# Kernel optimization log

Measured on AMD Instinct MI355X. Metric: run time of the kernel, lower is better.

The kernel has to match this reference:

```python
import jax, jax.numpy as jnp
import numpy as np

# Config constants (HNet300MConfig)
D = 1536          # d_model
H = 12            # n_heads // 2 used by chunk_attention
MAXC = 256        # max_chunks
MAXSEQ = 1024     # max_seq_length (size_embedding rows)
THRESH = 0.85     # boundary_threshold
B, S = 8, 1024


def setup_inputs() -> dict:
    key = jax.random.key(0)
    ks = jax.random.split(key, 10)
    def nrm(k, shape, scale=0.02):
        return jax.random.normal(k, shape, dtype=jnp.float32) * scale
    return {
        "x": jax.random.normal(ks[0], (B, S, D), dtype=jnp.float32),
        "boundaries": jax.random.uniform(ks[1], (B, S), dtype=jnp.float32),
        # nn.MultiheadAttention params
        "in_proj_w": nrm(ks[2], (3 * D, D)),
        "in_proj_b": jnp.zeros((3 * D,), jnp.float32),
        "out_w": nrm(ks[3], (D, D)),
        "out_b": jnp.zeros((D,), jnp.float32),
        # chunk_processor: Linear(D,2D) -> GELU -> Linear(2D,D) -> LayerNorm
        "w1": nrm(ks[4], (2 * D, D)),
        "b1": jnp.zeros((2 * D,), jnp.float32),
        "w2": nrm(ks[5], (D, 2 * D)),
        "b2": jnp.zeros((D,), jnp.float32),
        "ln_g": jnp.ones((D,), jnp.float32),
        "ln_b": jnp.zeros((D,), jnp.float32),
        "pos_enc": nrm(ks[6], (1, MAXC, D)),         # chunk_pos_encoding
        "size_emb": nrm(ks[7], (MAXSEQ, D), 1.0),    # size_embedding table
    }


def reference(x, boundaries, in_proj_w, in_proj_b, out_w, out_b,
              w1, b1, w2, b2, ln_g, ln_b, pos_enc, size_emb):
    dh = D // H
    # Chunk structure: boundary positions start chunks; seg_id = #boundaries up to
    # and including this token, minus 1. Tokens before the first boundary (seg=-1)
    # belong to no chunk. Final chunk runs from last boundary to seq end.
    is_b = boundaries > THRESH                                   # [B,S]
    seg = jnp.cumsum(is_b.astype(jnp.int32), axis=1) - 1         # [B,S]
    valid = seg >= 0

    # Per-chunk self-attention == full MHA with a block-diagonal mask.
    qkv = x @ in_proj_w.T + in_proj_b                            # [B,S,3D]
    q, k, v = jnp.split(qkv, 3, axis=-1)
    heads = lambda t: t.reshape(B, S, H, dh).transpose(0, 2, 1, 3)  # [B,H,S,dh]
    q, k, v = heads(q), heads(k), heads(v)
    scores = jnp.einsum('bhid,bhjd->bhij', q, k) / jnp.sqrt(jnp.float32(dh))
    blk = (seg[:, :, None] == seg[:, None, :]) & valid[:, :, None]  # [B,S,S]
    scores = jnp.where(blk[:, None], scores, jnp.float32(-1e9))
    attn = jax.nn.softmax(scores, axis=-1)
    ctx = jnp.einsum('bhij,bhjd->bhid', attn, v)
    ctx = ctx.transpose(0, 2, 1, 3).reshape(B, S, D)
    attn_out = ctx @ out_w.T + out_b                             # [B,S,D]

    # Ragged mean-pool per chunk (chunks beyond max_chunks are truncated;
    # tokens with seg=-1 or seg>=MAXC go to a dump bucket).
    seg_c = jnp.where(valid & (seg < MAXC), seg, MAXC)
    flat_seg = (seg_c + jnp.arange(B, dtype=jnp.int32)[:, None] * (MAXC + 1)).reshape(-1)
    sums = jax.ops.segment_sum(attn_out.reshape(-1, D), flat_seg,
                               num_segments=B * (MAXC + 1))
    cnts = jax.ops.segment_sum(jnp.ones((B * S,), jnp.float32), flat_seg,
                               num_segments=B * (MAXC + 1))
    sums = sums.reshape(B, MAXC + 1, D)[:, :MAXC]                # [B,MAXC,D]
    cnts = cnts.reshape(B, MAXC + 1)[:, :MAXC]                   # [B,MAXC]
    mean = sums / jnp.maximum(cnts, 1.0)[..., None]              # 0 for empty chunks

    # Size embedding added per non-empty chunk; empty (padding) chunks stay zero.
    lengths = cnts.astype(jnp.int32)
    size_idx = jnp.minimum(lengths, MAXSEQ - 1)
    size_vec = size_emb[size_idx] * (lengths > 0)[..., None].astype(jnp.float32)

    chunks = mean + size_vec + pos_enc                           # [B,MAXC,D]

    # chunk_processor (dropout inactive at inference)
    h = chunks @ w1.T + b1
    h = jax.nn.gelu(h, approximate=False)
    h = h @ w2.T + b2
    mu = jnp.mean(h, axis=-1, keepdims=True)
    var = jnp.mean((h - mu) ** 2, axis=-1, keepdims=True)
    out = (h - mu) / jnp.sqrt(var + 1e-5) * ln_g + ln_b
    return out
```

## Files before the change

kernel.cpp:

```cpp
#include <hip/hip_runtime.h>
#include <math.h>

#define NB 8
#define SEQ 1024
#define DM 1536
#define NHEAD 12
#define DHEAD 128
#define MAXC 256
#define QKVN 4608
#define THRESH 0.85f

typedef unsigned short u16;
typedef __attribute__((ext_vector_type(8))) __bf16 bf16x8;
typedef __attribute__((ext_vector_type(4))) float f32x4;

struct __align__(4) U2 { u16 x, y; };
struct __align__(8) U4 { u16 x, y, z, w; };

__device__ __forceinline__ float bf2f(u16 u) {
  union { unsigned i; float f; } c; c.i = ((unsigned)u) << 16; return c.f;
}
__device__ __forceinline__ u16 f2bf(float f) {
  union { float f; unsigned i; } c; c.f = f;
  unsigned r = c.i + 0x7FFFu + ((c.i >> 16) & 1u);
  return (u16)(r >> 16);
}

__global__ __launch_bounds__(256) void cvt5_bf16_kernel(
    const float* __restrict__ i0, u16* __restrict__ o0, int n0,
    const float* __restrict__ i1, u16* __restrict__ o1, int n1,
    const float* __restrict__ i2, u16* __restrict__ o2, int n2,
    const float* __restrict__ i3, u16* __restrict__ o3, int n3,
    const float* __restrict__ i4, u16* __restrict__ o4, int n4) {
  const int stride = gridDim.x * blockDim.x;
  const int t0 = blockIdx.x * blockDim.x + threadIdx.x;
  const float* ins[5] = {i0, i1, i2, i3, i4};
  u16* outs[5] = {o0, o1, o2, o3, o4};
  const int ns[5] = {n0, n1, n2, n3, n4};
#pragma unroll
  for (int a = 0; a < 5; ++a) {
    const float* in = ins[a];
    u16* out = outs[a];
    for (int i = t0; i < ns[a]; i += stride) {
      float4 f = ((const float4*)in)[i];
      U4 u; u.x = f2bf(f.x); u.y = f2bf(f.y); u.z = f2bf(f.z); u.w = f2bf(f.w);
      ((U4*)out)[i] = u;
    }
  }
}

__global__ __launch_bounds__(64) void segment_kernel(
    const float* __restrict__ bnd, int* __restrict__ nchunks,
    int* __restrict__ starts, int* __restrict__ lens) {
  const int b = blockIdx.x;
  const int lane = threadIdx.x;
  int running = 0;
  for (int g = 0; g < SEQ / 64; ++g) {
    int s = g * 64 + lane;
    bool isb = bnd[b * SEQ + s] > THRESH;
    unsigned long long mask = __ballot(isb ? 1 : 0);
    int excl = __popcll(mask & ((1ULL << lane) - 1ULL));
    if (isb) {
      int c = running + excl;
      if (c <= MAXC) starts[b * (MAXC + 1) + c] = s;
    }
    running += __popcll(mask);
  }
  if (lane == 0) nchunks[b] = running;
  __syncthreads();
  int ncl = min(running, MAXC);
  for (int c = lane; c < MAXC; c += 64) {
    int v = 0;
    if (c < ncl) {
      int st = starts[b * (MAXC + 1) + c];
      int en = (c + 1 < running) ? starts[b * (MAXC + 1) + c + 1] : SEQ;
      v = en - st;
    }
    lens[b * MAXC + c] = v;
  }
}

__global__ __launch_bounds__(512, 2) void gemm256_kernel(
    const u16* __restrict__ A, const u16* __restrict__ B,
    const int M, const int N, const int K,
    const float* __restrict__ bias, u16* __restrict__ outB) {
  __shared__ __align__(16) u16 lds[3][2][8192];
  const int tid = threadIdx.x;
  const int wid = tid >> 6;
  const int lane = tid & 63;
  const int cpx = gridDim.x >> 3;
  const int bid = ((int)blockIdx.x & 7) * cpx + ((int)blockIdx.x >> 3);
  const int NX = N >> 8;
  const int row0 = (bid / NX) << 8;
  const int col0 = (bid % NX) << 8;

  const int wr = wid >> 2;
  const int wc = wid & 3;
  const int rr = lane & 15;
  const int kg = lane >> 4;
  const int cw = rr * 4 + kg;
  const int slot = cw ^ ((cw >> 3) & 7);
  int srow[2], sk8[2];
#pragma unroll
  for (int i = 0; i < 2; ++i) {
    const int s = i * 512 + tid;
    const int g = s >> 6, c = s & 63;
    const int gch = c ^ ((c >> 3) & 7);
    srow[i] = g * 16 + (gch >> 2);
    sk8[i] = gch & 3;
  }

  const int NT = K >> 5;

#define STAGE_A(t)                                                            \
  {                                                                           \
    const int _b = (t) % 3;                                                   \
    const int _kb = (t) << 5;                                                 \
    _Pragma("unroll") for (int i = 0; i < 2; ++i) {                           \
      u16* ga = const_cast<u16*>(A) + (size_t)(row0 + srow[i]) * K + _kb +    \
                sk8[i] * 8;                                                   \
      __builtin_amdgcn_global_load_lds(                                       \
          (__attribute__((address_space(1))) void*)ga,                        \
          (__attribute__((address_space(3))) void*)&lds[_b][0]                \
              [(i * 512 + wid * 64) * 8], 16, 0, 0);                          \
    }                                                                         \
  }
#define STAGE_B(t)                                                            \
  {                                                                           \
    const int _b = (t) % 3;                                                   \
    const int _kb = (t) << 5;                                                 \
    _Pragma("unroll") for (int i = 0; i < 2; ++i) {                           \
      u16* gb = const_cast<u16*>(B) + (size_t)(col0 + srow[i]) * K + _kb +    \
                sk8[i] * 8;                                                   \
      __builtin_amdgcn_global_load_lds(                                       \
          (__attribute__((address_space(1))) void*)gb,                        \
          (__attribute__((address_space(3))) void*)&lds[_b][1]                \
              [(i * 512 + wid * 64) * 8], 16, 0, 0);                          \
    }                                                                         \
  }

  f32x4 acc[8][4] = {};

  STAGE_A(0); STAGE_B(0);
  STAGE_A(1); STAGE_B(1);
  asm volatile("s_waitcnt vmcnt(4)" ::: "memory");
  __builtin_amdgcn_s_barrier();

  for (int t = 0; t < NT; ++t) {
    const int buf = t % 3;
    bf16x8 af[8], bf[4];
#pragma unroll
    for (int m = 0; m < 8; ++m)
      af[m] = *(const bf16x8*)&lds[buf][0][((wr * 8 + m) * 64 + slot) * 8];
#pragma unroll
    for (int n = 0; n < 4; ++n)
      bf[n] = *(const bf16x8*)&lds[buf][1][((wc * 4 + n) * 64 + slot) * 8];
    if (t + 2 < NT) { STAGE_A(t + 2); STAGE_B(t + 2); }
    __builtin_amdgcn_s_barrier();
    asm volatile("s_waitcnt lgkmcnt(0)" ::: "memory");
    __builtin_amdgcn_sched_barrier(0);
    __builtin_amdgcn_s_setprio(1);
#pragma unroll
    for (int m = 0; m < 8; ++m)
#pragma unroll
      for (int n = 0; n < 4; ++n)
        acc[m][n] = __builtin_amdgcn_mfma_f32_16x16x32_bf16(af[m], bf[n], acc[m][n], 0, 0, 0);
    __builtin_amdgcn_s_setprio(0);
    if (t + 2 < NT) {
      asm volatile("s_waitcnt vmcnt(4)" ::: "memory");
    } else if (t + 1 < NT) {
      asm volatile("s_waitcnt vmcnt(0)" ::: "memory");
    }
    __builtin_amdgcn_s_barrier();
  }
#undef STAGE_A
#undef STAGE_B

#pragma unroll
  for (int m = 0; m < 8; ++m) {
#pragma unroll
    for (int n = 0; n < 4; ++n) {
      const int col = col0 + wc * 64 + n * 16 + rr;
      const float bs = bias[col];
#pragma unroll
      for (int j = 0; j < 4; ++j) {
        const int row = row0 + wr * 128 + m * 16 + (lane >> 4) * 4 + j;
        outB[(size_t)row * N + col] = f2bf(acc[m][n][j] + bs);
      }
    }
  }
}

template <int MODE>
__global__ __launch_bounds__(256) void gemm_bf16_kernel(
    const u16* __restrict__ A, const u16* __restrict__ B,
    const int M, const int N, const int K,
    const float* __restrict__ bias,
    u16* __restrict__ outB, float* __restrict__ outF,
    const int* __restrict__ lens, const float* __restrict__ semb,
    const float* __restrict__ pos) {
  __shared__ __align__(16) u16 As[128 * 32];
  __shared__ __align__(16) u16 Bs[128 * 32];
  const int tid = threadIdx.x;
  const int wave = tid >> 6;
  const int lane = tid & 63;
  const int row0 = blockIdx.y * 128;
  const int col0 = blockIdx.x * 128;
  const int wm = (wave >> 1) * 64;
  const int wn = (wave & 1) * 64;
  const int gch = lane ^ ((lane >> 3) & 7);
  const int sr = gch >> 2;
  const int sc = (gch & 3) * 8;
  const int rr = lane & 15;
  const int kg = lane >> 4;
  const int cwant = rr * 4 + kg;
  const int slot = cwant ^ ((cwant >> 3) & 7);
  f32x4 acc[4][4] = {};

  for (int k0 = 0; k0 < K; k0 += 32) {
    __syncthreads();
#pragma unroll
    for (int t = 0; t < 2; ++t) {
      const int li = wave * 2 + t;
      u16* ga = const_cast<u16*>(A) + (size_t)(row0 + li * 16 + sr) * K + (k0 + sc);
      u16* gb = const_cast<u16*>(B) + (size_t)(col0 + li * 16 + sr) * K + (k0 + sc);
      __builtin_amdgcn_global_load_lds(
          (__attribute__((address_space(1))) void*)ga,
          (__attribute__((address_space(3))) void*)(As + li * 512), 16, 0, 0);
      __builtin_amdgcn_global_load_lds(
          (__attribute__((address_space(1))) void*)gb,
          (__attribute__((address_space(3))) void*)(Bs + li * 512), 16, 0, 0);
    }
    __syncthreads();
    bf16x8 af[4], bfr[4];
#pragma unroll
    for (int m = 0; m < 4; ++m)
      af[m] = *(const bf16x8*)(As + ((wm >> 4) + m) * 512 + slot * 8);
#pragma unroll
    for (int n = 0; n < 4; ++n)
      bfr[n] = *(const bf16x8*)(Bs + ((wn >> 4) + n) * 512 + slot * 8);
#pragma unroll
    for (int m = 0; m < 4; ++m)
#pragma unroll
      for (int n = 0; n < 4; ++n)
        acc[m][n] = __builtin_amdgcn_mfma_f32_16x16x32_bf16(af[m], bfr[n], acc[m][n], 0, 0, 0);
  }

  const int rg = (lane >> 4) * 4;
#pragma unroll
  for (int m = 0; m < 4; ++m) {
#pragma unroll
    for (int n = 0; n < 4; ++n) {
      const int col = col0 + wn + n * 16 + rr;
#pragma unroll
      for (int j = 0; j < 4; ++j) {
        const int row = row0 + wm + m * 16 + rg + j;
        float v = acc[m][n][j];
        if (MODE == 2) {
          const int len = lens[row];
          float val = 0.f;
          if (len > 0) {
            const int si = len < 1023 ? len : 1023;
            val = v + bias[col] + semb[(size_t)si * DM + col];
          }
          val += pos[(size_t)(row & (MAXC - 1)) * DM + col];
          outB[(size_t)row * N + col] = f2bf(val);
        } else if (MODE == 3) {
          float z = v + bias[col];
          float gel = 0.5f * z * (1.f + erff(z * 0.70710678118654752440f));
          outB[(size_t)row * N + col] = f2bf(gel);
        } else {
          outF[(size_t)row * N + col] = v + bias[col];
        }
      }
    }
  }
}

__global__ __launch_bounds__(64) void chunk_attn_kernel(
    const u16* __restrict__ qkv, const int* __restrict__ nchunks,
    const int* __restrict__ starts, const int* __restrict__ lens,
    u16* __restrict__ pooled) {
  __shared__ float g_lds[SEQ];
  const int h = blockIdx.x;
  const int c = blockIdx.y;
  const int b = blockIdx.z;
  const int lane = threadIdx.x;
  const int nc = min(nchunks[b], MAXC);
  u16* prow = pooled + ((size_t)(b * MAXC + c)) * DM + h * DHEAD;
  if (c >= nc) {
    U2 z; z.x = 0; z.y = 0;
    *(U2*)(prow + lane * 2) = z;
    return;
  }
  const int s0 = starts[b * (MAXC + 1) + c];
  const int L = lens[b * MAXC + c];
  const u16* Qb = qkv + ((size_t)(b * SEQ + s0)) * QKVN + h * DHEAD;
  const u16* Kb = Qb + DM;
  const u16* Vb = Qb + 2 * DM;

  const int col = lane & 15;
  const int grp = lane >> 4;
  const float scale = 0.08838834764831845f;

  float a0 = 0.f, a1 = 0.f;

  if (L <= 16) {
    const int rc = col < L ? col : (L - 1);
    bf16x8 qf[4], kf[4];
#pragma unroll
    for (int s = 0; s < 4; ++s) {
      qf[s] = *(const bf16x8*)(Qb + (size_t)rc * QKVN + s * 32 + grp * 8);
      kf[s] = *(const bf16x8*)(Kb + (size_t)rc * QKVN + s * 32 + grp * 8);
    }
    f32x4 sc = {0.f, 0.f, 0.f, 0.f};
#pragma unroll
    for (int s = 0; s < 4; ++s)
      sc = __builtin_amdgcn_mfma_f32_16x16x32_bf16(qf[s], kf[s], sc, 0, 0, 0);
    const bool kvalid = col < L;
    float g = 0.f;
#pragma unroll
    for (int j = 0; j < 4; ++j) {
      float sj = sc[j] * scale;
      float mv = kvalid ? sj : -3e38f;
      mv = fmaxf(mv, __shfl_xor(mv, 1));
      mv = fmaxf(mv, __shfl_xor(mv, 2));
      mv = fmaxf(mv, __shfl_xor(mv, 4));
      mv = fmaxf(mv, __shfl_xor(mv, 8));
      float pv = kvalid ? __expf(sj - mv) : 0.f;
      float dv = pv;
      dv += __shfl_xor(dv, 1);
      dv += __shfl_xor(dv, 2);
      dv += __shfl_xor(dv, 4);
      dv += __shfl_xor(dv, 8);
      const bool rv = (grp * 4 + j) < L;
      g += rv ? pv / dv : 0.f;
    }
    g += __shfl_xor(g, 16);
    g += __shfl_xor(g, 32);
    for (int j = 0; j < L; ++j) {
      float gj = __shfl(g, j);
      U2 vv = *(const U2*)(Vb + (size_t)j * QKVN + lane * 2);
      a0 += gj * bf2f(vv.x);
      a1 += gj * bf2f(vv.y);
    }
  } else {
    float* gw = g_lds;
    for (int j = lane; j < L; j += 64) gw[j] = 0.f;
    const int NT = (L + 15) >> 4;
    for (int qt = 0; qt < NT; ++qt) {
      const int qr = qt * 16 + col;
      const int qrc = qr < L ? qr : (L - 1);
      bf16x8 qf[4];
#pragma unroll
      for (int s = 0; s < 4; ++s)
        qf[s] = *(const bf16x8*)(Qb + (size_t)qrc * QKVN + s * 32 + grp * 8);

      float m[4] = {-3e38f, -3e38f, -3e38f, -3e38f};
      float den[4] = {0.f, 0.f, 0.f, 0.f};
      for (int kt = 0; kt < NT; ++kt) {
        const int kr = kt * 16 + col;
        const bool kvalid = kr < L;
        const int krc = kvalid ? kr : (L - 1);
        f32x4 sc = {0.f, 0.f, 0.f, 0.f};
#pragma unroll
        for (int s = 0; s < 4; ++s) {
          bf16x8 kf = *(const bf16x8*)(Kb + (size_t)krc * QKVN + s * 32 + grp * 8);
          sc = __builtin_amdgcn_mfma_f32_16x16x32_bf16(qf[s], kf, sc, 0, 0, 0);
        }
#pragma unroll
        for (int j = 0; j < 4; ++j) {
          float sj = sc[j] * scale;
          float mv = kvalid ? sj : -3e38f;
          mv = fmaxf(mv, __shfl_xor(mv, 1));
          mv = fmaxf(mv, __shfl_xor(mv, 2));
          mv = fmaxf(mv, __shfl_xor(mv, 4));
          mv = fmaxf(mv, __shfl_xor(mv, 8));
          float mn = fmaxf(m[j], mv);
          float pv = kvalid ? __expf(sj - mn) : 0.f;
          pv += __shfl_xor(pv, 1);
          pv += __shfl_xor(pv, 2);
          pv += __shfl_xor(pv, 4);
          pv += __shfl_xor(pv, 8);
          den[j] = den[j] * __expf(m[j] - mn) + pv;
          m[j] = mn;
        }
      }
      float inv[4];
#pragma unroll
      for (int j = 0; j < 4; ++j) {
        const bool rv = (qt * 16 + grp * 4 + j) < L;
        inv[j] = rv ? 1.f / den[j] : 0.f;
      }
      for (int kt = 0; kt < NT; ++kt) {
        const int kr = kt * 16 + col;
        const bool kvalid = kr < L;
        const int krc = kvalid ? kr : (L - 1);
        f32x4 sc = {0.f, 0.f, 0.f, 0.f};
#pragma unroll
        for (int s = 0; s < 4; ++s) {
          bf16x8 kf = *(const bf16x8*)(Kb + (size_t)krc * QKVN + s * 32 + grp * 8);
          sc = __builtin_amdgcn_mfma_f32_16x16x32_bf16(qf[s], kf, sc, 0, 0, 0);
        }
        float colsum = 0.f;
#pragma unroll
        for (int j = 0; j < 4; ++j)
          colsum += __expf(sc[j] * scale - m[j]) * inv[j];
        colsum += __shfl_xor(colsum, 16);
        colsum += __shfl_xor(colsum, 32);
        if (grp == 0 && kvalid) gw[kt * 16 + col] += colsum;
      }
    }
    for (int j = 0; j < L; ++j) {
      float gj = gw[j];
      U2 vv = *(const U2*)(Vb + (size_t)j * QKVN + lane * 2);
      a0 += gj * bf2f(vv.x);
      a1 += gj * bf2f(vv.y);
    }
  }
  const float invL = 1.f / (float)L;
  U2 r; r.x = f2bf(a0 * invL); r.y = f2bf(a1 * invL);
  *(U2*)(prow + lane * 2) = r;
}

__global__ __launch_bounds__(256) void ln_kernel(
    const float* __restrict__ h2, const float* __restrict__ gamma,
    const float* __restrict__ beta, float* __restrict__ out) {
  const int row = blockIdx.x;
  const float* x = h2 + (size_t)row * DM;
  float* o = out + (size_t)row * DM;
  const int tid = threadIdx.x;
  float v[6];
  float s = 0.f;
#pragma unroll
  for (int i = 0; i < 6; ++i) { v[i] = x[tid + i * 256]; s += v[i]; }
  __shared__ float red[8];
#pragma unroll
  for (int off = 32; off; off >>= 1) s += __shfl_xor(s, off);
  if ((tid & 63) == 0) red[tid >> 6] = s;
  __syncthreads();
  const float mu = (red[0] + red[1] + red[2] + red[3]) * (1.f / (float)DM);
  float vs = 0.f;
#pragma unroll
  for (int i = 0; i < 6; ++i) { float d = v[i] - mu; vs += d * d; }
#pragma unroll
  for (int off = 32; off; off >>= 1) vs += __shfl_xor(vs, off);
  __shared__ float red2[8];
  if ((tid & 63) == 0) red2[tid >> 6] = vs;
  __syncthreads();
  const float var = (red2[0] + red2[1] + red2[2] + red2[3]) * (1.f / (float)DM);
  const float inv = rsqrtf(var + 1e-5f);
#pragma unroll
  for (int i = 0; i < 6; ++i) {
    const int cidx = tid + i * 256;
    o[cidx] = (v[i] - mu) * inv * gamma[cidx] + beta[cidx];
  }
}

extern "C" void kernel_launch(void* const* d_in, const int* in_sizes, int n_in,
                              void* d_out, int out_size, void* d_ws, size_t ws_size,
                              hipStream_t stream) {
  const float* x    = (const float*)d_in[0];
  const float* bnd  = (const float*)d_in[1];
  const float* wqkv = (const float*)d_in[2];
  const float* bqkv = (const float*)d_in[3];
  const float* wout = (const float*)d_in[4];
  const float* bout = (const float*)d_in[5];
  const float* w1   = (const float*)d_in[6];
  const float* b1   = (const float*)d_in[7];
  const float* w2   = (const float*)d_in[8];
  const float* b2   = (const float*)d_in[9];
  const float* lng  = (const float*)d_in[10];
  const float* lnb  = (const float*)d_in[11];
  const float* pos  = (const float*)d_in[12];
  const float* semb = (const float*)d_in[13];
  float* out = (float*)d_out;

  char* ws = (char*)d_ws;
  size_t off = 0;
  auto alloc = [&](size_t bytes) -> char* {
    char* p = ws + off;
    off += (bytes + 255) & ~(size_t)255;
    return p;
  };
  u16* x_bf    = (u16*)alloc((size_t)NB * SEQ * DM * 2);
  u16* wqkv_bf = (u16*)alloc((size_t)3 * DM * DM * 2);
  u16* wout_bf = (u16*)alloc((size_t)DM * DM * 2);
  u16* w1_bf   = (u16*)alloc((size_t)2 * DM * DM * 2);
  u16* w2_bf   = (u16*)alloc((size_t)2 * DM * DM * 2);
  u16* qkv_bf  = (u16*)alloc((size_t)NB * SEQ * QKVN * 2);
  int* nchunks = (int*)alloc(NB * 4);
  int* starts  = (int*)alloc(NB * (MAXC + 1) * 4);
  int* lens    = (int*)alloc(NB * MAXC * 4);
  u16* pooled  = (u16*)alloc((size_t)NB * MAXC * DM * 2);
  u16* chunks  = (u16*)alloc((size_t)NB * MAXC * DM * 2);
  u16* h1      = (u16*)alloc((size_t)NB * MAXC * 2 * DM * 2);
  float* h2    = (float*)alloc((size_t)NB * MAXC * DM * 4);
  (void)ws_size; (void)in_sizes; (void)n_in; (void)out_size;

  cvt5_bf16_kernel<<<2048, 256, 0, stream>>>(
      x, x_bf, NB * SEQ * DM / 4,
      wqkv, wqkv_bf, 3 * DM * DM / 4,
      wout, wout_bf, DM * DM / 4,
      w1, w1_bf, 2 * DM * DM / 4,
      w2, w2_bf, 2 * DM * DM / 4);

  segment_kernel<<<NB, 64, 0, stream>>>(bnd, nchunks, starts, lens);

  gemm256_kernel<<<(NB * SEQ / 256) * (QKVN / 256), 512, 0, stream>>>(
      x_bf, wqkv_bf, NB * SEQ, QKVN, DM, bqkv, qkv_bf);

  chunk_attn_kernel<<<dim3(NHEAD, MAXC, NB), 64, 0, stream>>>(
      qkv_bf, nchunks, starts, lens, pooled);

  gemm_bf16_kernel<2><<<dim3(DM / 128, NB * MAXC / 128), 256, 0, stream>>>(
      pooled, wout_bf, NB * MAXC, DM, DM, bout, chunks, nullptr, lens, semb, pos);

  gemm_bf16_kernel<3><<<dim3(2 * DM / 128, NB * MAXC / 128), 256, 0, stream>>>(
      chunks, w1_bf, NB * MAXC, 2 * DM, DM, b1, h1, nullptr, nullptr, nullptr, nullptr);

  gemm_bf16_kernel<4><<<dim3(DM / 128, NB * MAXC / 128), 256, 0, stream>>>(
      h1, w2_bf, NB * MAXC, DM, 2 * DM, b2, nullptr, h2, nullptr, nullptr, nullptr);

  ln_kernel<<<NB * MAXC, 256, 0, stream>>>(h2, lng, lnb, out);
}
```

Measured before the change: 396.4 us.

## Deepen GEMM prefetch pipelines and vectorize chunk-attention V accumulation

The 256-tile GEMM goes from three to four LDS stages with a prefetch distance of three and drops one barrier per iteration. The 128-tile GEMM gains double buffering so the next k-slab loads while MFMAs run. The chunk-attention V accumulation now has each half-wave take alternate rows with 4-wide loads, then combines the halves with a shuffle. LDS use rises (4x32KB per block in the 256 kernel), which may cut occupancy below the launch-bound target of 2 blocks, and removing the barrier may expose a reuse race on the buffer.

```diff
diff --git a/kernel.cpp b/kernel.cpp
--- a/kernel.cpp
+++ b/kernel.cpp
@@ -84,7 +84,7 @@
     const u16* __restrict__ A, const u16* __restrict__ B,
     const int M, const int N, const int K,
     const float* __restrict__ bias, u16* __restrict__ outB) {
-  __shared__ __align__(16) u16 lds[3][2][8192];
+  __shared__ __align__(16) u16 lds[4][2][8192];
   const int tid = threadIdx.x;
   const int wid = tid >> 6;
   const int lane = tid & 63;
@@ -112,26 +112,19 @@
 
   const int NT = K >> 5;
 
-#define STAGE_A(t)                                                            \
+#define STAGE(t)                                                              \
   {                                                                           \
-    const int _b = (t) % 3;                                                   \
+    const int _b = (t) & 3;                                                   \
     const int _kb = (t) << 5;                                                 \
     _Pragma("unroll") for (int i = 0; i < 2; ++i) {                           \
       u16* ga = const_cast<u16*>(A) + (size_t)(row0 + srow[i]) * K + _kb +    \
+                sk8[i] * 8;                                                   \
+      u16* gb = const_cast<u16*>(B) + (size_t)(col0 + srow[i]) * K + _kb +    \
                 sk8[i] * 8;                                                   \
       __builtin_amdgcn_global_load_lds(                                       \
           (__attribute__((address_space(1))) void*)ga,                        \
           (__attribute__((address_space(3))) void*)&lds[_b][0]                \
               [(i * 512 + wid * 64) * 8], 16, 0, 0);                          \
-    }                                                                         \
-  }
-#define STAGE_B(t)                                                            \
-  {                                                                           \
-    const int _b = (t) % 3;                                                   \
-    const int _kb = (t) << 5;                                                 \
-    _Pragma("unroll") for (int i = 0; i < 2; ++i) {                           \
-      u16* gb = const_cast<u16*>(B) + (size_t)(col0 + srow[i]) * K + _kb +    \
-                sk8[i] * 8;                                                   \
       __builtin_amdgcn_global_load_lds(                                       \
           (__attribute__((address_space(1))) void*)gb,                        \
           (__attribute__((address_space(3))) void*)&lds[_b][1]                \
@@ -141,13 +134,12 @@
 
   f32x4 acc[8][4] = {};
 
-  STAGE_A(0); STAGE_B(0);
-  STAGE_A(1); STAGE_B(1);
-  asm volatile("s_waitcnt vmcnt(4)" ::: "memory");
+  STAGE(0); STAGE(1); STAGE(2);
+  asm volatile("s_waitcnt vmcnt(8)" ::: "memory");
   __builtin_amdgcn_s_barrier();
 
   for (int t = 0; t < NT; ++t) {
-    const int buf = t % 3;
+    const int buf = t & 3;
     bf16x8 af[8], bf[4];
 #pragma unroll
     for (int m = 0; m < 8; ++m)
@@ -155,8 +147,7 @@
 #pragma unroll
     for (int n = 0; n < 4; ++n)
       bf[n] = *(const bf16x8*)&lds[buf][1][((wc * 4 + n) * 64 + slot) * 8];
-    if (t + 2 < NT) { STAGE_A(t + 2); STAGE_B(t + 2); }
-    __builtin_amdgcn_s_barrier();
+    if (t + 3 < NT) STAGE(t + 3);
     asm volatile("s_waitcnt lgkmcnt(0)" ::: "memory");
     __builtin_amdgcn_sched_barrier(0);
     __builtin_amdgcn_s_setprio(1);
@@ -166,15 +157,16 @@
       for (int n = 0; n < 4; ++n)
         acc[m][n] = __builtin_amdgcn_mfma_f32_16x16x32_bf16(af[m], bf[n], acc[m][n], 0, 0, 0);
     __builtin_amdgcn_s_setprio(0);
-    if (t + 2 < NT) {
+    if (t + 3 < NT) {
+      asm volatile("s_waitcnt vmcnt(8)" ::: "memory");
+    } else if (t + 2 < NT) {
       asm volatile("s_waitcnt vmcnt(4)" ::: "memory");
     } else if (t + 1 < NT) {
       asm volatile("s_waitcnt vmcnt(0)" ::: "memory");
     }
     __builtin_amdgcn_s_barrier();
   }
-#undef STAGE_A
-#undef STAGE_B
+#undef STAGE
 
 #pragma unroll
   for (int m = 0; m < 8; ++m) {
@@ -199,8 +191,8 @@
     u16* __restrict__ outB, float* __restrict__ outF,
     const int* __restrict__ lens, const float* __restrict__ semb,
     const float* __restrict__ pos) {
-  __shared__ __align__(16) u16 As[128 * 32];
-  __shared__ __align__(16) u16 Bs[128 * 32];
+  __shared__ __align__(16) u16 As[2][128 * 32];
+  __shared__ __align__(16) u16 Bs[2][128 * 32];
   const int tid = threadIdx.x;
   const int wave = tid >> 6;
   const int lane = tid & 63;
@@ -215,36 +207,54 @@
   const int kg = lane >> 4;
   const int cwant = rr * 4 + kg;
   const int slot = cwant ^ ((cwant >> 3) & 7);
+  const int NT = K >> 5;
   f32x4 acc[4][4] = {};
 
-  for (int k0 = 0; k0 < K; k0 += 32) {
-    __syncthreads();
-#pragma unroll
-    for (int t = 0; t < 2; ++t) {
-      const int li = wave * 2 + t;
-      u16* ga = const_cast<u16*>(A) + (size_t)(row0 + li * 16 + sr) * K + (k0 + sc);
-      u16* gb = const_cast<u16*>(B) + (size_t)(col0 + li * 16 + sr) * K + (k0 + sc);
-      __builtin_amdgcn_global_load_lds(
-          (__attribute__((address_space(1))) void*)ga,
-          (__attribute__((address_space(3))) void*)(As + li * 512), 16, 0, 0);
-      __builtin_amdgcn_global_load_lds(
-          (__attribute__((address_space(1))) void*)gb,
-          (__attribute__((address_space(3))) void*)(Bs + li * 512), 16, 0, 0);
-    }
-    __syncthreads();
+#define STAGE128(t, bb)                                                       \
+  {                                                                           \
+    const int _k = (t) << 5;                                                  \
+    _Pragma("unroll") for (int tt = 0; tt < 2; ++tt) {                        \
+      const int li = wave * 2 + tt;                                           \
+      u16* ga = const_cast<u16*>(A) + (size_t)(row0 + li * 16 + sr) * K +     \
+                _k + sc;                                                      \
+      u16* gb = const_cast<u16*>(B) + (size_t)(col0 + li * 16 + sr) * K +     \
+                _k + sc;                                                      \
+      __builtin_amdgcn_global_load_lds(                                       \
+          (__attribute__((address_space(1))) void*)ga,                        \
+          (__attribute__((address_space(3))) void*)(As[bb] + li * 512), 16,   \
+          0, 0);                                                              \
+      __builtin_amdgcn_global_load_lds(                                       \
+          (__attribute__((address_space(1))) void*)gb,                        \
+          (__attribute__((address_space(3))) void*)(Bs[bb] + li * 512), 16,   \
+          0, 0);                                                              \
+    }                                                                         \
+  }
+
+  STAGE128(0, 0);
+  asm volatile("s_waitcnt vmcnt(0)" ::: "memory");
+  __builtin_amdgcn_s_barrier();
+
+  for (int t = 0; t < NT; ++t) {
+    const int cb = t & 1;
     bf16x8 af[4], bfr[4];
 #pragma unroll
     for (int m = 0; m < 4; ++m)
-      af[m] = *(const bf16x8*)(As + ((wm >> 4) + m) * 512 + slot * 8);
+      af[m] = *(const bf16x8*)(As[cb] + ((wm >> 4) + m) * 512 + slot * 8);
 #pragma unroll
     for (int n = 0; n < 4; ++n)
-      bfr[n] = *(const bf16x8*)(Bs + ((wn >> 4) + n) * 512 + slot * 8);
+      bfr[n] = *(const bf16x8*)(Bs[cb] + ((wn >> 4) + n) * 512 + slot * 8);
+    if (t + 1 < NT) STAGE128(t + 1, cb ^ 1);
+    asm volatile("s_waitcnt lgkmcnt(0)" ::: "memory");
+    __builtin_amdgcn_sched_barrier(0);
 #pragma unroll
     for (int m = 0; m < 4; ++m)
 #pragma unroll
       for (int n = 0; n < 4; ++n)
         acc[m][n] = __builtin_amdgcn_mfma_f32_16x16x32_bf16(af[m], bfr[n], acc[m][n], 0, 0, 0);
-  }
+    if (t + 1 < NT) asm volatile("s_waitcnt vmcnt(0)" ::: "memory");
+    __builtin_amdgcn_s_barrier();
+  }
+#undef STAGE128
 
   const int rg = (lane >> 4) * 4;
 #pragma unroll
@@ -302,8 +312,10 @@
   const int col = lane & 15;
   const int grp = lane >> 4;
   const float scale = 0.08838834764831845f;
-
-  float a0 = 0.f, a1 = 0.f;
+  const int half = lane >> 5;
+  const int dl4 = (lane & 31) * 4;
+
+  float a[4] = {0.f, 0.f, 0.f, 0.f};
 
   if (L <= 16) {
     const int rc = col < L ? col : (L - 1);
@@ -338,11 +350,15 @@
     }
     g += __shfl_xor(g, 16);
     g += __shfl_xor(g, 32);
-    for (int j = 0; j < L; ++j) {
-      float gj = __shfl(g, j);
-      U2 vv = *(const U2*)(Vb + (size_t)j * QKVN + lane * 2);
-      a0 += gj * bf2f(vv.x);
-      a1 += gj * bf2f(vv.y);
+    for (int j = 0; j < L; j += 2) {
+      const int jj = j + half;
+      const bool jv = jj < L;
+      float gj = __shfl(g, jv ? jj : 0);
+      if (!jv) gj = 0.f;
+      const int jc = jv ? jj : 0;
+      U4 vv = *(const U4*)(Vb + (size_t)jc * QKVN + dl4);
+      a[0] += gj * bf2f(vv.x); a[1] += gj * bf2f(vv.y);
+      a[2] += gj * bf2f(vv.z); a[3] += gj * bf2f(vv.w);
     }
   } else {
     float* gw = g_lds;
@@ -411,16 +427,26 @@
         if (grp == 0 && kvalid) gw[kt * 16 + col] += colsum;
       }
     }
-    for (int j = 0; j < L; ++j) {
-      float gj = gw[j];
-      U2 vv = *(const U2*)(Vb + (size_t)j * QKVN + lane * 2);
-      a0 += gj * bf2f(vv.x);
-      a1 += gj * bf2f(vv.y);
+    for (int j = 0; j < L; j += 2) {
+      const int jj = j + half;
+      const bool jv = jj < L;
+      float gj = jv ? gw[jj] : 0.f;
+      const int jc = jv ? jj : 0;
+      U4 vv = *(const U4*)(Vb + (size_t)jc * QKVN + dl4);
+      a[0] += gj * bf2f(vv.x); a[1] += gj * bf2f(vv.y);
+      a[2] += gj * bf2f(vv.z); a[3] += gj * bf2f(vv.w);
     }
   }
   const float invL = 1.f / (float)L;
-  U2 r; r.x = f2bf(a0 * invL); r.y = f2bf(a1 * invL);
-  *(U2*)(prow + lane * 2) = r;
+#pragma unroll
+  for (int i = 0; i < 4; ++i) {
+    a[i] += __shfl_xor(a[i], 32);
+    a[i] *= invL;
+  }
+  if (lane < 32) {
+    U4 r; r.x = f2bf(a[0]); r.y = f2bf(a[1]); r.z = f2bf(a[2]); r.w = f2bf(a[3]);
+    *(U4*)(prow + dl4) = r;
+  }
 }
 
 __global__ __launch_bounds__(256) void ln_kernel(
```

Measured after the change: 353.4 us. -10.9%, faster.
